# Performance work log

Hardware: AMD Instinct MI355X
Metric: run time of the kernel (lower is better)

Reference implementation:

```python
import jax, jax.numpy as jnp
import numpy as np

B, S, D, F, E = 8, 2048, 512, 2048, 8


def setup_inputs() -> dict:
    key = jax.random.key(0)
    ks = jax.random.split(key, 7)
    x = jax.random.normal(ks[0], (B, S, D), dtype=jnp.float32)
    Wr = jax.random.normal(ks[1], (D, E), dtype=jnp.float32) * 0.02
    br = jnp.zeros((E,), dtype=jnp.float32)
    W1 = jax.random.normal(ks[2], (E, D, F), dtype=jnp.float32) * 0.02
    b1 = jnp.zeros((E, F), dtype=jnp.float32)
    W2 = jax.random.normal(ks[3], (E, F, D), dtype=jnp.float32) * 0.02
    b2 = jnp.zeros((E, D), dtype=jnp.float32)
    return {"x": x, "Wr": Wr, "br": br, "W1": W1, "b1": b1, "W2": W2, "b2": b2}


def reference(x, Wr, br, W1, b1, W2, b2):
    # Router: softmax gate + top-2
    logits = jnp.einsum('bsd,de->bse', x, Wr) + br            # [B,S,E]
    gate = jax.nn.softmax(logits, axis=-1)                    # [B,S,E]
    top2_val, top2_idx = jax.lax.top_k(gate, 2)               # [B,S,2]

    # Combine weights: gate value on the two selected experts, 0 elsewhere
    onehot = jax.nn.one_hot(top2_idx, E, dtype=x.dtype)       # [B,S,2,E]
    combine = jnp.sum(onehot * top2_val[..., None], axis=2)   # [B,S,E]

    # Dense per-expert FFN, masked-combined (same math as the token loop)
    out = jnp.zeros_like(x)
    for e in range(E):
        h = jax.nn.relu(jnp.einsum('bsd,df->bsf', x, W1[e]) + b1[e])
        y = jnp.einsum('bsf,fd->bsd', h, W2[e]) + b2[e]
        out = out + combine[..., e, None] * y

    # GShard-style load-balancing aux loss
    expert_prob = gate.mean(axis=(0, 1))                      # [E]
    aux_loss = jnp.sum(expert_prob * jnp.log(expert_prob + 1e-9))
    return out, aux_loss
```

## Files before the change

kernel.cpp:

```cpp
#include <hip/hip_runtime.h>
#include <math.h>

typedef unsigned short u16;
typedef __attribute__((ext_vector_type(8))) short short8;
typedef __attribute__((ext_vector_type(8))) u16 u16x8;
typedef __attribute__((ext_vector_type(4))) float f32x4;

#define NTOK 16384
#define DDIM 512
#define FDIM 2048
#define ENUM 8
#define NBLK 1024
#define APAD (32768 + 256)
#define MAXTILES 264

__device__ __forceinline__ u16 f2bf(float f) {
  unsigned u = __float_as_uint(f);
  u += 0x7FFFu + ((u >> 16) & 1u);
  return (u16)(u >> 16);
}
__device__ __forceinline__ float bf2f(u16 b) {
  return __uint_as_float(((unsigned)b) << 16);
}

typedef const __attribute__((address_space(1))) unsigned int* gas1_t;
typedef __attribute__((address_space(3))) unsigned int* las3_t;
__device__ __forceinline__ void gload16(const u16* g, u16* l) {
  __builtin_amdgcn_global_load_lds((gas1_t)(const void*)g, (las3_t)(void*)l, 16, 0, 0);
}

__global__ __launch_bounds__(256) void router_kernel(
    const float* __restrict__ x, const float* __restrict__ Wr,
    const float* __restrict__ br, int* __restrict__ top2e,
    float* __restrict__ top2v, int* __restrict__ histBase,
    float* __restrict__ gatePart) {
  __shared__ __align__(16) float sWr[DDIM * ENUM];
  __shared__ __align__(16) float sX[4][DDIM];
  __shared__ int sHist[ENUM];
  __shared__ float sGate[ENUM];
  int tid = threadIdx.x;
  for (int i = tid; i < DDIM * ENUM; i += 256) sWr[i] = Wr[i];
  if (tid < ENUM) { sHist[tid] = 0; sGate[tid] = 0.f; }
  __syncthreads();
  int wave = tid >> 6, lane = tid & 63;
  int e = lane >> 3, dg = lane & 7;
  float bre = br[e];
  for (int it = 0; it < 4; ++it) {
    int t = blockIdx.x * 16 + wave * 4 + it;
    const float4* xr = (const float4*)(x + (size_t)t * DDIM);
    float4* sx4 = (float4*)sX[wave];
    sx4[lane] = xr[lane];
    sx4[lane + 64] = xr[lane + 64];
    asm volatile("s_waitcnt lgkmcnt(0)" ::: "memory");
    float acc = 0.f;
#pragma unroll 16
    for (int i = 0; i < 64; ++i) {
      float xv = sX[wave][i * 8 + dg];
      acc += xv * sWr[(i * 8 + dg) * 8 + e];
    }
    acc += __shfl_xor(acc, 1);
    acc += __shfl_xor(acc, 2);
    acc += __shfl_xor(acc, 4);
    float logit = acc + bre;
    float m = logit;
    m = fmaxf(m, __shfl_xor(m, 8));
    m = fmaxf(m, __shfl_xor(m, 16));
    m = fmaxf(m, __shfl_xor(m, 32));
    float pv = expf(logit - m);
    float s = pv;
    s += __shfl_xor(s, 8);
    s += __shfl_xor(s, 16);
    s += __shfl_xor(s, 32);
    float gate = pv / s;
    float v1 = gate; int i1 = e;
#pragma unroll
    for (int msk = 8; msk <= 32; msk <<= 1) {
      float ov = __shfl_xor(v1, msk);
      int oi = __shfl_xor(i1, msk);
      if (ov > v1 || (ov == v1 && oi < i1)) { v1 = ov; i1 = oi; }
    }
    float g2 = (e == i1) ? -1.f : gate;
    float v2 = g2; int i2 = e;
#pragma unroll
    for (int msk = 8; msk <= 32; msk <<= 1) {
      float ov = __shfl_xor(v2, msk);
      int oi = __shfl_xor(i2, msk);
      if (ov > v2 || (ov == v2 && oi < i2)) { v2 = ov; i2 = oi; }
    }
    if (lane == 0) {
      top2e[2 * t] = i1; top2e[2 * t + 1] = i2;
      top2v[2 * t] = v1; top2v[2 * t + 1] = v2;
      atomicAdd(&sHist[i1], 1);
      atomicAdd(&sHist[i2], 1);
    }
    if (dg == 0) atomicAdd(&sGate[e], gate);
  }
  __syncthreads();
  if (tid < ENUM) {
    histBase[blockIdx.x * 8 + tid] = sHist[tid];
    gatePart[blockIdx.x * 8 + tid] = sGate[tid];
  }
}

__global__ __launch_bounds__(256) void scan_kernel(
    int* __restrict__ histBase, const float* __restrict__ gatePart,
    int* __restrict__ offsets, int* __restrict__ counts,
    int* __restrict__ tileE, int* __restrict__ tileM, int* __restrict__ nTiles,
    float* __restrict__ auxOut) {
  __shared__ int sTot[ENUM];
  __shared__ float sG[ENUM];
  int tid = threadIdx.x, wave = tid >> 6, lane = tid & 63;
  if (tid < ENUM) sG[tid] = 0.f;
  __syncthreads();
  float loc[8] = {0, 0, 0, 0, 0, 0, 0, 0};
  for (int r = tid; r < NBLK; r += 256) {
#pragma unroll
    for (int e = 0; e < 8; ++e) loc[e] += gatePart[r * 8 + e];
  }
#pragma unroll
  for (int e = 0; e < 8; ++e) atomicAdd(&sG[e], loc[e]);
#pragma unroll
  for (int ei = 0; ei < 2; ++ei) {
    int e = wave * 2 + ei;
    int running = 0;
    for (int itb = 0; itb < NBLK / 64; ++itb) {
      int idx = (itb * 64 + lane) * 8 + e;
      int v = histBase[idx];
      int inc = v;
#pragma unroll
      for (int d = 1; d < 64; d <<= 1) {
        int o = __shfl_up(inc, d);
        if (lane >= d) inc += o;
      }
      histBase[idx] = running + inc - v;
      running += __shfl(inc, 63);
    }
    if (lane == 0) sTot[e] = running;
  }
  __syncthreads();
  if (tid == 0) {
    int off = 0, nt = 0;
#pragma unroll
    for (int e = 0; e < 8; ++e) {
      int c = sTot[e];
      offsets[e] = off; counts[e] = c; off += c;
      int mt = (c + 127) >> 7;
      for (int m = 0; m < mt; ++m) { tileE[nt] = e; tileM[nt] = m; ++nt; }
    }
    *nTiles = nt;
    float aux = 0.f;
#pragma unroll
    for (int e = 0; e < 8; ++e) {
      float pr = sG[e] / (float)NTOK;
      aux += pr * logf(pr + 1e-9f);
    }
    *auxOut = aux;
  }
}

__global__ __launch_bounds__(256) void place_kernel(
    const float* __restrict__ x, const int* __restrict__ top2e,
    const float* __restrict__ top2v, const int* __restrict__ histBase,
    const int* __restrict__ offsets, int* __restrict__ tokA,
    float* __restrict__ assignW, u16* __restrict__ Xg) {
  __shared__ int sA[32];
  int tid = threadIdx.x, wave = tid >> 6, lane = tid & 63;
  int blk = blockIdx.x;
  if (tid < 32) {
    int slot = tid;
    int t = blk * 16 + (slot >> 1);
    int e = top2e[2 * t + (slot & 1)];
    float v = top2v[2 * t + (slot & 1)];
    int rank = 0;
#pragma unroll
    for (int ee = 0; ee < 8; ++ee) {
      unsigned long long mm = __ballot(e == ee);
      if (e == ee) rank = __popcll(mm & ((1ull << slot) - 1));
    }
    int a = offsets[e] + histBase[blk * 8 + e] + rank;
    sA[slot] = a;
    tokA[2 * t + (slot & 1)] = a;
    assignW[a] = v;
  }
  __syncthreads();
  for (int it = 0; it < 4; ++it) {
    int lt = wave * 4 + it;
    int t = blk * 16 + lt;
    const float4* xr = (const float4*)(x + (size_t)t * DDIM);
    float4 v0 = xr[lane * 2], v1 = xr[lane * 2 + 1];
    u16x8 o;
    o[0] = f2bf(v0.x); o[1] = f2bf(v0.y); o[2] = f2bf(v0.z); o[3] = f2bf(v0.w);
    o[4] = f2bf(v1.x); o[5] = f2bf(v1.y); o[6] = f2bf(v1.z); o[7] = f2bf(v1.w);
    int a1 = sA[2 * lt], a2 = sA[2 * lt + 1];
    *(u16x8*)(Xg + (size_t)a1 * DDIM + lane * 8) = o;
    *(u16x8*)(Xg + (size_t)a2 * DDIM + lane * 8) = o;
  }
}

__global__ __launch_bounds__(256) void transpose_kernel(
    const float* __restrict__ W, u16* __restrict__ WT, int K, int N) {
  __shared__ float tile[64][65];
  int e = blockIdx.y;
  int tn_count = N >> 6;
  int tk = blockIdx.x / tn_count;
  int tn = blockIdx.x - tk * tn_count;
  const float* Wp = W + (size_t)e * K * N;
  u16* WTp = WT + (size_t)e * N * K;
  int c = threadIdx.x & 63, r = threadIdx.x >> 6;
#pragma unroll
  for (int i = 0; i < 16; ++i) {
    int row = r + i * 4;
    tile[row][c] = Wp[(size_t)(tk * 64 + row) * N + tn * 64 + c];
  }
  __syncthreads();
#pragma unroll
  for (int i = 0; i < 16; ++i) {
    int row = r + i * 4;
    WTp[(size_t)(tn * 64 + row) * K + tk * 64 + c] = f2bf(tile[c][row]);
  }
}

template <int K>
__device__ __forceinline__ void gemm_mainloop(const u16* __restrict__ A,
                                              const u16* __restrict__ B,
                                              u16* As, u16* Bs,
                                              f32x4 (&acc)[4][4]) {
  int tid = threadIdx.x;
  int wave = tid >> 6, lane = tid & 63;
  int wr = wave >> 1, wc = wave & 1;
  int c0 = tid, c1 = tid + 256;
  int r0 = c0 >> 2, r1 = c1 >> 2;
  int f0 = (r0 ^ (r0 >> 2)) & 3;
  int k0c = ((c0 & 3) ^ f0) * 8;
  int k1c = ((c1 & 3) ^ f0) * 8;
  const u16* Ag0 = A + (size_t)r0 * K + k0c;
  const u16* Ag1 = A + (size_t)r1 * K + k1c;
  const u16* Bg0 = B + (size_t)r0 * K + k0c;
  const u16* Bg1 = B + (size_t)r1 * K + k1c;
  int wb = wave * 512;
  int fr = lane & 15;
  int sw = (fr ^ (fr >> 2)) & 3;
  int slot = (lane >> 4) ^ sw;
  int fA = (wr * 64 + fr) * 32 + slot * 8;
  int fB = (wc * 64 + fr) * 32 + slot * 8;

  gload16(Ag0, As + wb);
  gload16(Ag1, As + 2048 + wb);
  gload16(Bg0, Bs + wb);
  gload16(Bg1, Bs + 2048 + wb);
  __syncthreads();
  int cur = 0;
  for (int k0 = 32; k0 < K; k0 += 32) {
    int nb = (cur ^ 1) * 4096;
    gload16(Ag0 + k0, As + nb + wb);
    gload16(Ag1 + k0, As + nb + 2048 + wb);
    gload16(Bg0 + k0, Bs + nb + wb);
    gload16(Bg1 + k0, Bs + nb + 2048 + wb);
    const u16* Ac = As + cur * 4096;
    const u16* Bc = Bs + cur * 4096;
    short8 af[4], bf[4];
#pragma unroll
    for (int m = 0; m < 4; ++m) af[m] = *(const short8*)(Ac + fA + m * 512);
#pragma unroll
    for (int n = 0; n < 4; ++n) bf[n] = *(const short8*)(Bc + fB + n * 512);
#pragma unroll
    for (int m = 0; m < 4; ++m)
#pragma unroll
      for (int n = 0; n < 4; ++n)
        acc[m][n] = __builtin_amdgcn_mfma_f32_16x16x32_bf16(af[m], bf[n],
                                                            acc[m][n], 0, 0, 0);
    __syncthreads();
    cur ^= 1;
  }
  const u16* Ac = As + cur * 4096;
  const u16* Bc = Bs + cur * 4096;
  short8 af[4], bf[4];
#pragma unroll
  for (int m = 0; m < 4; ++m) af[m] = *(const short8*)(Ac + fA + m * 512);
#pragma unroll
  for (int n = 0; n < 4; ++n) bf[n] = *(const short8*)(Bc + fB + n * 512);
#pragma unroll
  for (int m = 0; m < 4; ++m)
#pragma unroll
    for (int n = 0; n < 4; ++n)
      acc[m][n] = __builtin_amdgcn_mfma_f32_16x16x32_bf16(af[m], bf[n],
                                                          acc[m][n], 0, 0, 0);
}

__global__ __launch_bounds__(256) void gemm1_kernel(
    const u16* __restrict__ Xg, const u16* __restrict__ W1T,
    const float* __restrict__ b1, u16* __restrict__ h,
    const int* __restrict__ counts, const int* __restrict__ offsets,
    const int* __restrict__ tileE, const int* __restrict__ tileM,
    const int* __restrict__ nTiles) {
  if ((int)blockIdx.x >= *nTiles) return;
  int e = tileE[blockIdx.x], mtile = tileM[blockIdx.x];
  int ntile = blockIdx.y;
  int cnt = counts[e], off = offsets[e];
  const u16* A = Xg + (size_t)(off + mtile * 128) * DDIM;
  const u16* B = W1T + ((size_t)e * FDIM + ntile * 128) * DDIM;
  __shared__ __align__(16) u16 As[2 * 128 * 32];
  __shared__ __align__(16) u16 Bs[2 * 128 * 32];
  f32x4 acc[4][4] = {};
  gemm_mainloop<DDIM>(A, B, As, Bs, acc);
  int lane = threadIdx.x & 63, wave = threadIdx.x >> 6;
  int wr = wave >> 1, wc = wave & 1;
  int cl = lane & 15, rq = (lane >> 4) * 4;
#pragma unroll
  for (int m = 0; m < 4; ++m) {
#pragma unroll
    for (int i = 0; i < 4; ++i) {
      int gr = mtile * 128 + wr * 64 + m * 16 + rq + i;
      if (gr < cnt) {
#pragma unroll
        for (int n = 0; n < 4; ++n) {
          int gc = ntile * 128 + wc * 64 + n * 16 + cl;
          float v = acc[m][n][i] + b1[e * FDIM + gc];
          v = fmaxf(v, 0.f);
          h[(size_t)(off + gr) * FDIM + gc] = f2bf(v);
        }
      }
    }
  }
}

__global__ __launch_bounds__(256) void gemm2_kernel(
    const u16* __restrict__ h, const u16* __restrict__ W2T,
    const float* __restrict__ b2, const float* __restrict__ assignW,
    const int* __restrict__ counts, const int* __restrict__ offsets,
    const int* __restrict__ tileE, const int* __restrict__ tileM,
    const int* __restrict__ nTiles, u16* __restrict__ z) {
  if ((int)blockIdx.x >= *nTiles) return;
  int e = tileE[blockIdx.x], mtile = tileM[blockIdx.x];
  int ntile = blockIdx.y;
  int cnt = counts[e], off = offsets[e];
  const u16* A = h + (size_t)(off + mtile * 128) * FDIM;
  const u16* B = W2T + ((size_t)e * DDIM + ntile * 128) * FDIM;
  __shared__ __align__(16) u16 As[2 * 128 * 32];
  __shared__ __align__(16) u16 Bs[2 * 128 * 32];
  f32x4 acc[4][4] = {};
  gemm_mainloop<FDIM>(A, B, As, Bs, acc);
  int lane = threadIdx.x & 63, wave = threadIdx.x >> 6;
  int wr = wave >> 1, wc = wave & 1;
  int cl = lane & 15, rq = (lane >> 4) * 4;
#pragma unroll
  for (int m = 0; m < 4; ++m) {
#pragma unroll
    for (int i = 0; i < 4; ++i) {
      int gr = mtile * 128 + wr * 64 + m * 16 + rq + i;
      if (gr < cnt) {
        int a = off + gr;
        float w = assignW[a];
#pragma unroll
        for (int n = 0; n < 4; ++n) {
          int gc = ntile * 128 + wc * 64 + n * 16 + cl;
          float v = (acc[m][n][i] + b2[e * DDIM + gc]) * w;
          z[(size_t)a * DDIM + gc] = f2bf(v);
        }
      }
    }
  }
}

__global__ __launch_bounds__(256) void combine_kernel(
    const u16* __restrict__ z, const int* __restrict__ tokA,
    float* __restrict__ out) {
  int tid = threadIdx.x, wave = tid >> 6, lane = tid & 63;
  int t = blockIdx.x * 4 + wave;
  int a1 = tokA[2 * t], a2 = tokA[2 * t + 1];
  u16x8 v1 = *(const u16x8*)(z + (size_t)a1 * DDIM + lane * 8);
  u16x8 v2 = *(const u16x8*)(z + (size_t)a2 * DDIM + lane * 8);
  float4 o0, o1;
  o0.x = bf2f(v1[0]) + bf2f(v2[0]);
  o0.y = bf2f(v1[1]) + bf2f(v2[1]);
  o0.z = bf2f(v1[2]) + bf2f(v2[2]);
  o0.w = bf2f(v1[3]) + bf2f(v2[3]);
  o1.x = bf2f(v1[4]) + bf2f(v2[4]);
  o1.y = bf2f(v1[5]) + bf2f(v2[5]);
  o1.z = bf2f(v1[6]) + bf2f(v2[6]);
  o1.w = bf2f(v1[7]) + bf2f(v2[7]);
  float4* o = (float4*)(out + (size_t)t * DDIM + lane * 8);
  o[0] = o0;
  o[1] = o1;
}

extern "C" void kernel_launch(void* const* d_in, const int* in_sizes, int n_in,
                              void* d_out, int out_size, void* d_ws, size_t ws_size,
                              hipStream_t stream) {
  const float* x  = (const float*)d_in[0];
  const float* Wr = (const float*)d_in[1];
  const float* br = (const float*)d_in[2];
  const float* W1 = (const float*)d_in[3];
  const float* b1 = (const float*)d_in[4];
  const float* W2 = (const float*)d_in[5];
  const float* b2 = (const float*)d_in[6];
  float* out = (float*)d_out;

  char* ws = (char*)d_ws;
  size_t p = 0;
  auto alloc = [&](size_t bytes) -> void* {
    void* r = ws + p;
    p = (p + bytes + 255) & ~(size_t)255;
    return r;
  };
  int* counts     = (int*)alloc(ENUM * 4);
  int* offsets    = (int*)alloc(ENUM * 4);
  int* nTiles     = (int*)alloc(4);
  int* tileE      = (int*)alloc(MAXTILES * 4);
  int* tileM      = (int*)alloc(MAXTILES * 4);
  int* top2e      = (int*)alloc((size_t)NTOK * 2 * 4);
  float* top2v    = (float*)alloc((size_t)NTOK * 2 * 4);
  int* tokA       = (int*)alloc((size_t)NTOK * 2 * 4);
  float* assignW  = (float*)alloc((size_t)APAD * 4);
  int* histBase   = (int*)alloc((size_t)NBLK * 8 * 4);
  float* gatePart = (float*)alloc((size_t)NBLK * 8 * 4);
  u16* W1T        = (u16*)alloc((size_t)ENUM * FDIM * DDIM * 2);
  u16* W2T        = (u16*)alloc((size_t)ENUM * DDIM * FDIM * 2);
  u16* Xg         = (u16*)alloc((size_t)APAD * DDIM * 2);
  u16* hbuf       = (u16*)alloc((size_t)APAD * FDIM * 2);
  u16* z          = Xg;
  (void)in_sizes; (void)n_in; (void)out_size; (void)ws_size;

  transpose_kernel<<<dim3(256, 8), 256, 0, stream>>>(W1, W1T, DDIM, FDIM);
  transpose_kernel<<<dim3(256, 8), 256, 0, stream>>>(W2, W2T, FDIM, DDIM);
  router_kernel<<<NBLK, 256, 0, stream>>>(x, Wr, br, top2e, top2v, histBase,
                                          gatePart);
  scan_kernel<<<1, 256, 0, stream>>>(histBase, gatePart, offsets, counts,
                                     tileE, tileM, nTiles,
                                     out + (size_t)NTOK * DDIM);
  place_kernel<<<NBLK, 256, 0, stream>>>(x, top2e, top2v, histBase, offsets,
                                         tokA, assignW, Xg);
  gemm1_kernel<<<dim3(MAXTILES, 16), 256, 0, stream>>>(
      Xg, W1T, b1, hbuf, counts, offsets, tileE, tileM, nTiles);
  gemm2_kernel<<<dim3(MAXTILES, 4), 256, 0, stream>>>(
      hbuf, W2T, b2, assignW, counts, offsets, tileE, tileM, nTiles, z);
  combine_kernel<<<NTOK / 4, 256, 0, stream>>>(z, tokA, out);
}
```

Before: 348.0 us.

## Rewrite expert GEMMs as 256x256 tiles with 8-wave ping-pong pipelined mainloop

Replaces the 128x128 double-buffered GEMM mainloop with a 256x256 tile kernel using 512 threads and 128KB of dynamic LDS. The new loop is a phased schedule: it splits A and B into K-halves, interleaves global-to-LDS loads with MFMA bursts, and uses explicit barriers, waitcnt and setprio to overlap memory with compute. Each tile's operands are reused more and there are fewer blocks. The cost is more padding waste for experts whose token counts are not multiples of 256, fewer blocks to fill the CUs, and one block per CU.

New measurement: 327.8 us. 5.8% less time.

```diff
diff --git a/kernel.cpp b/kernel.cpp
--- a/kernel.cpp
+++ b/kernel.cpp
@@ -12,7 +12,7 @@
 #define ENUM 8
 #define NBLK 1024
 #define APAD (32768 + 256)
-#define MAXTILES 264
+#define MAXT 144
 
 __device__ __forceinline__ u16 f2bf(float f) {
   unsigned u = __float_as_uint(f);
@@ -144,7 +144,7 @@
     for (int e = 0; e < 8; ++e) {
       int c = sTot[e];
       offsets[e] = off; counts[e] = c; off += c;
-      int mt = (c + 127) >> 7;
+      int mt = (c + 255) >> 8;
       for (int m = 0; m < mt; ++m) { tileE[nt] = e; tileM[nt] = m; ++nt; }
     }
     *nTiles = nt;
@@ -220,102 +220,120 @@
   }
 }
 
+
+#define STG(SP0, SP1, SOP, SBUF, SKH, SKT)                                     \
+  do {                                                                         \
+    const size_t go_ = (size_t)(SKT) * 64 + (SKH) * 32;                        \
+    gload16((SP0) + go_, (u16*)(ldsB + (SOP) * 65536 + (SBUF) * 32768 +        \
+                                (SKH) * 16384 + w1024));                       \
+    gload16((SP1) + go_, (u16*)(ldsB + (SOP) * 65536 + (SBUF) * 32768 +        \
+                                (SKH) * 16384 + 8192 + w1024));                \
+  } while (0)
+
+#define PH(MH, KS, CBUF, SP0, SP1, SOP, SBUF, SKH, SKT, GATE)                  \
+  do {                                                                         \
+    short8 areg[4];                                                            \
+    _Pragma("unroll")                                                          \
+    for (int m_ = 0; m_ < 4; ++m_)                                             \
+      areg[m_] = *(const short8*)(ldsB + (CBUF) * 32768 + (KS) * 16384 +       \
+                                  (MH) * 4096 + m_ * 1024 + frA);              \
+    if ((MH) == 0) {                                                           \
+      _Pragma("unroll")                                                        \
+      for (int n_ = 0; n_ < 4; ++n_)                                           \
+        breg[n_] = *(const short8*)(ldsB + 65536 + (CBUF) * 32768 +            \
+                                    (KS) * 16384 + n_ * 1024 + frB);           \
+    }                                                                          \
+    STG(SP0, SP1, SOP, SBUF, SKH, SKT);                                        \
+    if (GATE) asm volatile("s_waitcnt vmcnt(8)" ::: "memory");                 \
+    __builtin_amdgcn_s_barrier();                                              \
+    __builtin_amdgcn_sched_barrier(0);                                         \
+    __builtin_amdgcn_s_setprio(1);                                             \
+    _Pragma("unroll")                                                          \
+    for (int m_ = 0; m_ < 4; ++m_)                                             \
+      _Pragma("unroll")                                                        \
+      for (int n_ = 0; n_ < 4; ++n_)                                           \
+        acc[(MH) * 4 + m_][n_] = __builtin_amdgcn_mfma_f32_16x16x32_bf16(      \
+            areg[m_], breg[n_], acc[(MH) * 4 + m_][n_], 0, 0, 0);              \
+    __builtin_amdgcn_s_setprio(0);                                             \
+    __builtin_amdgcn_s_barrier();                                              \
+    __builtin_amdgcn_sched_barrier(0);                                         \
+  } while (0)
+
 template <int K>
-__device__ __forceinline__ void gemm_mainloop(const u16* __restrict__ A,
-                                              const u16* __restrict__ B,
-                                              u16* As, u16* Bs,
-                                              f32x4 (&acc)[4][4]) {
-  int tid = threadIdx.x;
-  int wave = tid >> 6, lane = tid & 63;
-  int wr = wave >> 1, wc = wave & 1;
-  int c0 = tid, c1 = tid + 256;
-  int r0 = c0 >> 2, r1 = c1 >> 2;
-  int f0 = (r0 ^ (r0 >> 2)) & 3;
-  int k0c = ((c0 & 3) ^ f0) * 8;
-  int k1c = ((c1 & 3) ^ f0) * 8;
-  const u16* Ag0 = A + (size_t)r0 * K + k0c;
-  const u16* Ag1 = A + (size_t)r1 * K + k1c;
-  const u16* Bg0 = B + (size_t)r0 * K + k0c;
-  const u16* Bg1 = B + (size_t)r1 * K + k1c;
-  int wb = wave * 512;
-  int fr = lane & 15;
-  int sw = (fr ^ (fr >> 2)) & 3;
-  int slot = (lane >> 4) ^ sw;
-  int fA = (wr * 64 + fr) * 32 + slot * 8;
-  int fB = (wc * 64 + fr) * 32 + slot * 8;
-
-  gload16(Ag0, As + wb);
-  gload16(Ag1, As + 2048 + wb);
-  gload16(Bg0, Bs + wb);
-  gload16(Bg1, Bs + 2048 + wb);
-  __syncthreads();
-  int cur = 0;
-  for (int k0 = 32; k0 < K; k0 += 32) {
-    int nb = (cur ^ 1) * 4096;
-    gload16(Ag0 + k0, As + nb + wb);
-    gload16(Ag1 + k0, As + nb + 2048 + wb);
-    gload16(Bg0 + k0, Bs + nb + wb);
-    gload16(Bg1 + k0, Bs + nb + 2048 + wb);
-    const u16* Ac = As + cur * 4096;
-    const u16* Bc = Bs + cur * 4096;
-    short8 af[4], bf[4];
-#pragma unroll
-    for (int m = 0; m < 4; ++m) af[m] = *(const short8*)(Ac + fA + m * 512);
-#pragma unroll
-    for (int n = 0; n < 4; ++n) bf[n] = *(const short8*)(Bc + fB + n * 512);
-#pragma unroll
-    for (int m = 0; m < 4; ++m)
-#pragma unroll
-      for (int n = 0; n < 4; ++n)
-        acc[m][n] = __builtin_amdgcn_mfma_f32_16x16x32_bf16(af[m], bf[n],
-                                                            acc[m][n], 0, 0, 0);
-    __syncthreads();
-    cur ^= 1;
-  }
-  const u16* Ac = As + cur * 4096;
-  const u16* Bc = Bs + cur * 4096;
-  short8 af[4], bf[4];
-#pragma unroll
-  for (int m = 0; m < 4; ++m) af[m] = *(const short8*)(Ac + fA + m * 512);
-#pragma unroll
-  for (int n = 0; n < 4; ++n) bf[n] = *(const short8*)(Bc + fB + n * 512);
-#pragma unroll
-  for (int m = 0; m < 4; ++m)
-#pragma unroll
-    for (int n = 0; n < 4; ++n)
-      acc[m][n] = __builtin_amdgcn_mfma_f32_16x16x32_bf16(af[m], bf[n],
-                                                          acc[m][n], 0, 0, 0);
-}
-
-__global__ __launch_bounds__(256) void gemm1_kernel(
+__device__ __forceinline__ void mainloop8(const u16* __restrict__ A,
+                                          const u16* __restrict__ B,
+                                          char* ldsB, f32x4 (&acc)[8][4]) {
+  const int tid = threadIdx.x;
+  const int lane = tid & 63, wave = tid >> 6;
+  const int wr = wave >> 2, wc = wave & 3;
+  const int fr = lane & 15;
+  const int swzRd = (((lane >> 4) ^ ((lane >> 1) & 3)) & 3) * 16;
+  const int frA = (wr * 128 + fr) * 64 + swzRd;
+  const int frB = (wc * 64 + fr) * 64 + swzRd;
+  const int w1024 = wave * 1024;
+  const int rowS = wave * 16 + (lane >> 2);
+  const int cswz = ((lane & 3) ^ ((lane >> 3) & 3)) * 8;
+  const u16* bA0 = A + (size_t)rowS * K + cswz;
+  const u16* bA1 = A + (size_t)(rowS + 128) * K + cswz;
+  const u16* bB0 = B + (size_t)rowS * K + cswz;
+  const u16* bB1 = B + (size_t)(rowS + 128) * K + cswz;
+  const int KT = K / 64, NIT = KT / 2;
+  short8 breg[4];
+
+  STG(bA0, bA1, 0, 0, 0, 0);
+  STG(bB0, bB1, 1, 0, 0, 0);
+  STG(bA0, bA1, 0, 0, 1, 0);
+  STG(bB0, bB1, 1, 0, 1, 0);
+  STG(bA0, bA1, 0, 1, 0, 1);
+  STG(bB0, bB1, 1, 1, 0, 1);
+  asm volatile("s_waitcnt vmcnt(8)" ::: "memory");
+  __builtin_amdgcn_s_barrier();
+  __builtin_amdgcn_sched_barrier(0);
+
+#pragma unroll 1
+  for (int it = 0; it < NIT; ++it) {
+    const int t1 = 2 * it + 1;
+    const int t2 = (2 * it + 2) & (KT - 1);
+    const int t3 = (2 * it + 3) & (KT - 1);
+    PH(0, 0, 0, bA0, bA1, 0, 1, 1, t1, 0);
+    PH(1, 0, 0, bB0, bB1, 1, 1, 1, t1, 1);
+    PH(0, 1, 0, bA0, bA1, 0, 0, 0, t2, 0);
+    PH(1, 1, 0, bB0, bB1, 1, 0, 0, t2, 1);
+    PH(0, 0, 1, bA0, bA1, 0, 0, 1, t2, 0);
+    PH(1, 0, 1, bB0, bB1, 1, 0, 1, t2, 1);
+    PH(0, 1, 1, bA0, bA1, 0, 1, 0, t3, 0);
+    PH(1, 1, 1, bB0, bB1, 1, 1, 0, t3, 1);
+  }
+}
+
+__global__ __launch_bounds__(512, 1) void gemm1_kernel(
     const u16* __restrict__ Xg, const u16* __restrict__ W1T,
     const float* __restrict__ b1, u16* __restrict__ h,
     const int* __restrict__ counts, const int* __restrict__ offsets,
     const int* __restrict__ tileE, const int* __restrict__ tileM,
     const int* __restrict__ nTiles) {
+  extern __shared__ char ldsB[];
   if ((int)blockIdx.x >= *nTiles) return;
   int e = tileE[blockIdx.x], mtile = tileM[blockIdx.x];
   int ntile = blockIdx.y;
   int cnt = counts[e], off = offsets[e];
-  const u16* A = Xg + (size_t)(off + mtile * 128) * DDIM;
-  const u16* B = W1T + ((size_t)e * FDIM + ntile * 128) * DDIM;
-  __shared__ __align__(16) u16 As[2 * 128 * 32];
-  __shared__ __align__(16) u16 Bs[2 * 128 * 32];
-  f32x4 acc[4][4] = {};
-  gemm_mainloop<DDIM>(A, B, As, Bs, acc);
+  const u16* A = Xg + (size_t)(off + mtile * 256) * DDIM;
+  const u16* B = W1T + ((size_t)e * FDIM + ntile * 256) * DDIM;
+  f32x4 acc[8][4] = {};
+  mainloop8<DDIM>(A, B, ldsB, acc);
   int lane = threadIdx.x & 63, wave = threadIdx.x >> 6;
-  int wr = wave >> 1, wc = wave & 1;
+  int wr = wave >> 2, wc = wave & 3;
   int cl = lane & 15, rq = (lane >> 4) * 4;
 #pragma unroll
-  for (int m = 0; m < 4; ++m) {
+  for (int ai = 0; ai < 8; ++ai) {
 #pragma unroll
     for (int i = 0; i < 4; ++i) {
-      int gr = mtile * 128 + wr * 64 + m * 16 + rq + i;
+      int gr = mtile * 256 + wr * 128 + ai * 16 + rq + i;
       if (gr < cnt) {
 #pragma unroll
         for (int n = 0; n < 4; ++n) {
-          int gc = ntile * 128 + wc * 64 + n * 16 + cl;
-          float v = acc[m][n][i] + b1[e * FDIM + gc];
+          int gc = ntile * 256 + wc * 64 + n * 16 + cl;
+          float v = acc[ai][n][i] + b1[e * FDIM + gc];
           v = fmaxf(v, 0.f);
           h[(size_t)(off + gr) * FDIM + gc] = f2bf(v);
         }
@@ -324,37 +342,36 @@
   }
 }
 
-__global__ __launch_bounds__(256) void gemm2_kernel(
+__global__ __launch_bounds__(512, 1) void gemm2_kernel(
     const u16* __restrict__ h, const u16* __restrict__ W2T,
     const float* __restrict__ b2, const float* __restrict__ assignW,
     const int* __restrict__ counts, const int* __restrict__ offsets,
     const int* __restrict__ tileE, const int* __restrict__ tileM,
     const int* __restrict__ nTiles, u16* __restrict__ z) {
+  extern __shared__ char ldsB[];
   if ((int)blockIdx.x >= *nTiles) return;
   int e = tileE[blockIdx.x], mtile = tileM[blockIdx.x];
   int ntile = blockIdx.y;
   int cnt = counts[e], off = offsets[e];
-  const u16* A = h + (size_t)(off + mtile * 128) * FDIM;
-  const u16* B = W2T + ((size_t)e * DDIM + ntile * 128) * FDIM;
-  __shared__ __align__(16) u16 As[2 * 128 * 32];
-  __shared__ __align__(16) u16 Bs[2 * 128 * 32];
-  f32x4 acc[4][4] = {};
-  gemm_mainloop<FDIM>(A, B, As, Bs, acc);
+  const u16* A = h + (size_t)(off + mtile * 256) * FDIM;
+  const u16* B = W2T + ((size_t)e * DDIM + ntile * 256) * FDIM;
+  f32x4 acc[8][4] = {};
+  mainloop8<FDIM>(A, B, ldsB, acc);
   int lane = threadIdx.x & 63, wave = threadIdx.x >> 6;
-  int wr = wave >> 1, wc = wave & 1;
+  int wr = wave >> 2, wc = wave & 3;
   int cl = lane & 15, rq = (lane >> 4) * 4;
 #pragma unroll
-  for (int m = 0; m < 4; ++m) {
+  for (int ai = 0; ai < 8; ++ai) {
 #pragma unroll
     for (int i = 0; i < 4; ++i) {
-      int gr = mtile * 128 + wr * 64 + m * 16 + rq + i;
+      int gr = mtile * 256 + wr * 128 + ai * 16 + rq + i;
       if (gr < cnt) {
         int a = off + gr;
         float w = assignW[a];
 #pragma unroll
         for (int n = 0; n < 4; ++n) {
-          int gc = ntile * 128 + wc * 64 + n * 16 + cl;
-          float v = (acc[m][n][i] + b2[e * DDIM + gc]) * w;
+          int gc = ntile * 256 + wc * 64 + n * 16 + cl;
+          float v = (acc[ai][n][i] + b2[e * DDIM + gc]) * w;
           z[(size_t)a * DDIM + gc] = f2bf(v);
         }
       }
@@ -406,8 +423,8 @@
   int* counts     = (int*)alloc(ENUM * 4);
   int* offsets    = (int*)alloc(ENUM * 4);
   int* nTiles     = (int*)alloc(4);
-  int* tileE      = (int*)alloc(MAXTILES * 4);
-  int* tileM      = (int*)alloc(MAXTILES * 4);
+  int* tileE      = (int*)alloc(MAXT * 4);
+  int* tileM      = (int*)alloc(MAXT * 4);
   int* top2e      = (int*)alloc((size_t)NTOK * 2 * 4);
   float* top2v    = (float*)alloc((size_t)NTOK * 2 * 4);
   int* tokA       = (int*)alloc((size_t)NTOK * 2 * 4);
@@ -421,6 +438,11 @@
   u16* z          = Xg;
   (void)in_sizes; (void)n_in; (void)out_size; (void)ws_size;
 
+  (void)hipFuncSetAttribute((const void*)gemm1_kernel,
+                            hipFuncAttributeMaxDynamicSharedMemorySize, 131072);
+  (void)hipFuncSetAttribute((const void*)gemm2_kernel,
+                            hipFuncAttributeMaxDynamicSharedMemorySize, 131072);
+
   transpose_kernel<<<dim3(256, 8), 256, 0, stream>>>(W1, W1T, DDIM, FDIM);
   transpose_kernel<<<dim3(256, 8), 256, 0, stream>>>(W2, W2T, FDIM, DDIM);
   router_kernel<<<NBLK, 256, 0, stream>>>(x, Wr, br, top2e, top2v, histBase,
@@ -430,9 +452,9 @@
                                      out + (size_t)NTOK * DDIM);
   place_kernel<<<NBLK, 256, 0, stream>>>(x, top2e, top2v, histBase, offsets,
                                          tokA, assignW, Xg);
-  gemm1_kernel<<<dim3(MAXTILES, 16), 256, 0, stream>>>(
+  gemm1_kernel<<<dim3(MAXT, 8), 512, 131072, stream>>>(
       Xg, W1T, b1, hbuf, counts, offsets, tileE, tileM, nTiles);
-  gemm2_kernel<<<dim3(MAXTILES, 4), 256, 0, stream>>>(
+  gemm2_kernel<<<dim3(MAXT, 2), 512, 131072, stream>>>(
       hbuf, W2T, b2, assignW, counts, offsets, tileE, tileM, nTiles, z);
   combine_kernel<<<NTOK / 4, 256, 0, stream>>>(z, tokA, out);
 }
```

## Widen GEMM tiles to 128x256 with 8 waves, remap grid, fuse transposes

Applied to the files above, without the earlier changes.

Both expert GEMMs now use 512-thread workgroups computing 128x256 output tiles, so each A tile in LDS is reused across twice as many columns and fewer A loads are issued overall. The 2D grid becomes a 1D grid with an XCD-aware block remap, MFMA sections are wrapped in s_setprio, and launch bounds request higher occupancy. The two weight-transpose launches are merged into one kernel using float4 loads and 16-byte bf16 stores. The trade-off is larger LDS per block and more wasted columns or threads on partially filled expert tiles.

Result: slower. 1.181 ms (+239.3%).

```diff
diff --git a/kernel.cpp b/kernel.cpp
--- a/kernel.cpp
+++ b/kernel.cpp
@@ -12,7 +12,9 @@
 #define ENUM 8
 #define NBLK 1024
 #define APAD (32768 + 256)
-#define MAXTILES 264
+#define NTCAP 264
+#define G1GRID 2112
+#define G2GRID 528
 
 __device__ __forceinline__ u16 f2bf(float f) {
   unsigned u = __float_as_uint(f);
@@ -105,7 +107,7 @@
 __global__ __launch_bounds__(256) void scan_kernel(
     int* __restrict__ histBase, const float* __restrict__ gatePart,
     int* __restrict__ offsets, int* __restrict__ counts,
-    int* __restrict__ tileE, int* __restrict__ tileM, int* __restrict__ nTiles,
+    int* __restrict__ tileE, int* __restrict__ tileM, int* __restrict__ nT,
     float* __restrict__ auxOut) {
   __shared__ int sTot[ENUM];
   __shared__ float sG[ENUM];
@@ -147,7 +149,7 @@
       int mt = (c + 127) >> 7;
       for (int m = 0; m < mt; ++m) { tileE[nt] = e; tileM[nt] = m; ++nt; }
     }
-    *nTiles = nt;
+    nT[0] = nt;
     float aux = 0.f;
 #pragma unroll
     for (int e = 0; e < 8; ++e) {
@@ -198,113 +200,125 @@
 }
 
 __global__ __launch_bounds__(256) void transpose_kernel(
-    const float* __restrict__ W, u16* __restrict__ WT, int K, int N) {
+    const float* __restrict__ W1, const float* __restrict__ W2,
+    u16* __restrict__ W1T, u16* __restrict__ W2T) {
   __shared__ float tile[64][65];
-  int e = blockIdx.y;
-  int tn_count = N >> 6;
-  int tk = blockIdx.x / tn_count;
-  int tn = blockIdx.x - tk * tn_count;
-  const float* Wp = W + (size_t)e * K * N;
-  u16* WTp = WT + (size_t)e * N * K;
-  int c = threadIdx.x & 63, r = threadIdx.x >> 6;
-#pragma unroll
-  for (int i = 0; i < 16; ++i) {
-    int row = r + i * 4;
-    tile[row][c] = Wp[(size_t)(tk * 64 + row) * N + tn * 64 + c];
-  }
-  __syncthreads();
-#pragma unroll
-  for (int i = 0; i < 16; ++i) {
-    int row = r + i * 4;
-    WTp[(size_t)(tn * 64 + row) * K + tk * 64 + c] = f2bf(tile[c][row]);
+  int q = threadIdx.x;
+  int half = blockIdx.y >> 3, e = blockIdx.y & 7;
+  const float* W = half ? W2 : W1;
+  u16* WT = half ? W2T : W1T;
+  int K = half ? FDIM : DDIM, N = half ? DDIM : FDIM;
+  int tnc = N >> 6;
+  int tk = blockIdx.x / tnc, tn = blockIdx.x - tk * tnc;
+  const float* Wp = W + (size_t)e * K * N + (size_t)(tk * 64) * N + tn * 64;
+#pragma unroll
+  for (int i = 0; i < 4; ++i) {
+    int row = (q >> 4) + i * 16, c4 = (q & 15) * 4;
+    float4 v = *(const float4*)(Wp + (size_t)row * N + c4);
+    tile[row][c4] = v.x; tile[row][c4 + 1] = v.y;
+    tile[row][c4 + 2] = v.z; tile[row][c4 + 3] = v.w;
+  }
+  __syncthreads();
+  u16* WTp = WT + (size_t)e * N * K + (size_t)(tn * 64) * K + tk * 64;
+#pragma unroll
+  for (int p = 0; p < 2; ++p) {
+    int n = (q >> 3) + p * 32, k0 = (q & 7) * 8;
+    u16x8 o;
+#pragma unroll
+    for (int j = 0; j < 8; ++j) o[j] = f2bf(tile[k0 + j][n]);
+    *(u16x8*)(WTp + (size_t)n * K + k0) = o;
   }
 }
 
 template <int K>
-__device__ __forceinline__ void gemm_mainloop(const u16* __restrict__ A,
-                                              const u16* __restrict__ B,
-                                              u16* As, u16* Bs,
-                                              f32x4 (&acc)[4][4]) {
-  int tid = threadIdx.x;
-  int wave = tid >> 6, lane = tid & 63;
-  int wr = wave >> 1, wc = wave & 1;
-  int c0 = tid, c1 = tid + 256;
-  int r0 = c0 >> 2, r1 = c1 >> 2;
-  int f0 = (r0 ^ (r0 >> 2)) & 3;
-  int k0c = ((c0 & 3) ^ f0) * 8;
-  int k1c = ((c1 & 3) ^ f0) * 8;
-  const u16* Ag0 = A + (size_t)r0 * K + k0c;
-  const u16* Ag1 = A + (size_t)r1 * K + k1c;
-  const u16* Bg0 = B + (size_t)r0 * K + k0c;
-  const u16* Bg1 = B + (size_t)r1 * K + k1c;
-  int wb = wave * 512;
-  int fr = lane & 15;
-  int sw = (fr ^ (fr >> 2)) & 3;
-  int slot = (lane >> 4) ^ sw;
-  int fA = (wr * 64 + fr) * 32 + slot * 8;
-  int fB = (wc * 64 + fr) * 32 + slot * 8;
-
-  gload16(Ag0, As + wb);
-  gload16(Ag1, As + 2048 + wb);
-  gload16(Bg0, Bs + wb);
-  gload16(Bg1, Bs + 2048 + wb);
-  __syncthreads();
+__device__ __forceinline__ void mainloopS(const u16* __restrict__ A,
+                                          const u16* __restrict__ B,
+                                          u16* As, u16* Bs,
+                                          f32x4 (&acc)[4][4]) {
+  const int tid = threadIdx.x;
+  const int lane = tid & 63, wave = tid >> 6;
+  const int wr = wave >> 2, wc = wave & 3;
+  const int fr = lane & 15;
+  const int slot = ((lane >> 4) ^ (fr ^ (fr >> 2))) & 3;
+  const int frA = (wr * 64 + fr) * 32 + slot * 8;
+  const int frB = (wc * 64 + fr) * 32 + slot * 8;
+  const int rA = tid >> 2;
+  const int sA = (((tid & 3) ^ (rA ^ (rA >> 2))) & 3) * 8;
+  const u16* Ag = A + (size_t)rA * K + sA;
+  const u16* Bg0 = B + (size_t)rA * K + sA;
+  const u16* Bg1 = B + (size_t)(rA + 128) * K + sA;
+  u16* Adst = As + wave * 512;
+  u16* Bdst0 = Bs + wave * 512;
+  u16* Bdst1 = Bs + 4096 + wave * 512;
+  const int KT = K / 32;
+
+  gload16(Ag, Adst);
+  gload16(Bg0, Bdst0);
+  gload16(Bg1, Bdst1);
+  __syncthreads();
+
   int cur = 0;
-  for (int k0 = 32; k0 < K; k0 += 32) {
-    int nb = (cur ^ 1) * 4096;
-    gload16(Ag0 + k0, As + nb + wb);
-    gload16(Ag1 + k0, As + nb + 2048 + wb);
-    gload16(Bg0 + k0, Bs + nb + wb);
-    gload16(Bg1 + k0, Bs + nb + 2048 + wb);
+#pragma unroll 1
+  for (int ks = 0; ks < KT - 1; ++ks) {
+    const int nb = cur ^ 1;
+    gload16(Ag + (ks + 1) * 32, Adst + nb * 4096);
+    gload16(Bg0 + (ks + 1) * 32, Bdst0 + nb * 8192);
+    gload16(Bg1 + (ks + 1) * 32, Bdst1 + nb * 8192);
     const u16* Ac = As + cur * 4096;
-    const u16* Bc = Bs + cur * 4096;
+    const u16* Bc = Bs + cur * 8192;
     short8 af[4], bf[4];
 #pragma unroll
-    for (int m = 0; m < 4; ++m) af[m] = *(const short8*)(Ac + fA + m * 512);
-#pragma unroll
-    for (int n = 0; n < 4; ++n) bf[n] = *(const short8*)(Bc + fB + n * 512);
+    for (int m = 0; m < 4; ++m) af[m] = *(const short8*)(Ac + frA + m * 512);
+#pragma unroll
+    for (int n = 0; n < 4; ++n) bf[n] = *(const short8*)(Bc + frB + n * 512);
+    __builtin_amdgcn_s_setprio(1);
 #pragma unroll
     for (int m = 0; m < 4; ++m)
 #pragma unroll
       for (int n = 0; n < 4; ++n)
         acc[m][n] = __builtin_amdgcn_mfma_f32_16x16x32_bf16(af[m], bf[n],
                                                             acc[m][n], 0, 0, 0);
+    __builtin_amdgcn_s_setprio(0);
     __syncthreads();
-    cur ^= 1;
-  }
-  const u16* Ac = As + cur * 4096;
-  const u16* Bc = Bs + cur * 4096;
-  short8 af[4], bf[4];
-#pragma unroll
-  for (int m = 0; m < 4; ++m) af[m] = *(const short8*)(Ac + fA + m * 512);
-#pragma unroll
-  for (int n = 0; n < 4; ++n) bf[n] = *(const short8*)(Bc + fB + n * 512);
-#pragma unroll
-  for (int m = 0; m < 4; ++m)
-#pragma unroll
-    for (int n = 0; n < 4; ++n)
-      acc[m][n] = __builtin_amdgcn_mfma_f32_16x16x32_bf16(af[m], bf[n],
-                                                          acc[m][n], 0, 0, 0);
-}
-
-__global__ __launch_bounds__(256) void gemm1_kernel(
+    cur = nb;
+  }
+  {
+    const u16* Ac = As + cur * 4096;
+    const u16* Bc = Bs + cur * 8192;
+    short8 af[4], bf[4];
+#pragma unroll
+    for (int m = 0; m < 4; ++m) af[m] = *(const short8*)(Ac + frA + m * 512);
+#pragma unroll
+    for (int n = 0; n < 4; ++n) bf[n] = *(const short8*)(Bc + frB + n * 512);
+#pragma unroll
+    for (int m = 0; m < 4; ++m)
+#pragma unroll
+      for (int n = 0; n < 4; ++n)
+        acc[m][n] = __builtin_amdgcn_mfma_f32_16x16x32_bf16(af[m], bf[n],
+                                                            acc[m][n], 0, 0, 0);
+  }
+}
+
+__global__ __launch_bounds__(512, 6) void gemm1_kernel(
     const u16* __restrict__ Xg, const u16* __restrict__ W1T,
     const float* __restrict__ b1, u16* __restrict__ h,
     const int* __restrict__ counts, const int* __restrict__ offsets,
     const int* __restrict__ tileE, const int* __restrict__ tileM,
-    const int* __restrict__ nTiles) {
-  if ((int)blockIdx.x >= *nTiles) return;
-  int e = tileE[blockIdx.x], mtile = tileM[blockIdx.x];
-  int ntile = blockIdx.y;
+    const int* __restrict__ nT) {
+  __shared__ __align__(16) u16 As[2 * 128 * 32];
+  __shared__ __align__(16) u16 Bs[2 * 256 * 32];
+  int wg = blockIdx.x;
+  int L = (wg & 7) * (G1GRID / 8) + (wg >> 3);
+  int tile = L >> 3, ntile = L & 7;
+  if (tile >= nT[0]) return;
+  int e = tileE[tile], mtile = tileM[tile];
   int cnt = counts[e], off = offsets[e];
   const u16* A = Xg + (size_t)(off + mtile * 128) * DDIM;
-  const u16* B = W1T + ((size_t)e * FDIM + ntile * 128) * DDIM;
-  __shared__ __align__(16) u16 As[2 * 128 * 32];
-  __shared__ __align__(16) u16 Bs[2 * 128 * 32];
+  const u16* B = W1T + ((size_t)e * FDIM + ntile * 256) * DDIM;
   f32x4 acc[4][4] = {};
-  gemm_mainloop<DDIM>(A, B, As, Bs, acc);
+  mainloopS<DDIM>(A, B, As, Bs, acc);
   int lane = threadIdx.x & 63, wave = threadIdx.x >> 6;
-  int wr = wave >> 1, wc = wave & 1;
+  int wr = wave >> 2, wc = wave & 3;
   int cl = lane & 15, rq = (lane >> 4) * 4;
 #pragma unroll
   for (int m = 0; m < 4; ++m) {
@@ -314,7 +328,7 @@
       if (gr < cnt) {
 #pragma unroll
         for (int n = 0; n < 4; ++n) {
-          int gc = ntile * 128 + wc * 64 + n * 16 + cl;
+          int gc = ntile * 256 + wc * 64 + n * 16 + cl;
           float v = acc[m][n][i] + b1[e * FDIM + gc];
           v = fmaxf(v, 0.f);
           h[(size_t)(off + gr) * FDIM + gc] = f2bf(v);
@@ -324,24 +338,26 @@
   }
 }
 
-__global__ __launch_bounds__(256) void gemm2_kernel(
+__global__ __launch_bounds__(512, 6) void gemm2_kernel(
     const u16* __restrict__ h, const u16* __restrict__ W2T,
     const float* __restrict__ b2, const float* __restrict__ assignW,
     const int* __restrict__ counts, const int* __restrict__ offsets,
     const int* __restrict__ tileE, const int* __restrict__ tileM,
-    const int* __restrict__ nTiles, u16* __restrict__ z) {
-  if ((int)blockIdx.x >= *nTiles) return;
-  int e = tileE[blockIdx.x], mtile = tileM[blockIdx.x];
-  int ntile = blockIdx.y;
+    const int* __restrict__ nT, u16* __restrict__ z) {
+  __shared__ __align__(16) u16 As[2 * 128 * 32];
+  __shared__ __align__(16) u16 Bs[2 * 256 * 32];
+  int wg = blockIdx.x;
+  int L = (wg & 7) * (G2GRID / 8) + (wg >> 3);
+  int tile = L >> 1, ntile = L & 1;
+  if (tile >= nT[0]) return;
+  int e = tileE[tile], mtile = tileM[tile];
   int cnt = counts[e], off = offsets[e];
   const u16* A = h + (size_t)(off + mtile * 128) * FDIM;
-  const u16* B = W2T + ((size_t)e * DDIM + ntile * 128) * FDIM;
-  __shared__ __align__(16) u16 As[2 * 128 * 32];
-  __shared__ __align__(16) u16 Bs[2 * 128 * 32];
+  const u16* B = W2T + ((size_t)e * DDIM + ntile * 256) * FDIM;
   f32x4 acc[4][4] = {};
-  gemm_mainloop<FDIM>(A, B, As, Bs, acc);
+  mainloopS<FDIM>(A, B, As, Bs, acc);
   int lane = threadIdx.x & 63, wave = threadIdx.x >> 6;
-  int wr = wave >> 1, wc = wave & 1;
+  int wr = wave >> 2, wc = wave & 3;
   int cl = lane & 15, rq = (lane >> 4) * 4;
 #pragma unroll
   for (int m = 0; m < 4; ++m) {
@@ -353,7 +369,7 @@
         float w = assignW[a];
 #pragma unroll
         for (int n = 0; n < 4; ++n) {
-          int gc = ntile * 128 + wc * 64 + n * 16 + cl;
+          int gc = ntile * 256 + wc * 64 + n * 16 + cl;
           float v = (acc[m][n][i] + b2[e * DDIM + gc]) * w;
           z[(size_t)a * DDIM + gc] = f2bf(v);
         }
@@ -405,9 +421,9 @@
   };
   int* counts     = (int*)alloc(ENUM * 4);
   int* offsets    = (int*)alloc(ENUM * 4);
-  int* nTiles     = (int*)alloc(4);
-  int* tileE      = (int*)alloc(MAXTILES * 4);
-  int* tileM      = (int*)alloc(MAXTILES * 4);
+  int* nT         = (int*)alloc(4);
+  int* tileE      = (int*)alloc(NTCAP * 4);
+  int* tileM      = (int*)alloc(NTCAP * 4);
   int* top2e      = (int*)alloc((size_t)NTOK * 2 * 4);
   float* top2v    = (float*)alloc((size_t)NTOK * 2 * 4);
   int* tokA       = (int*)alloc((size_t)NTOK * 2 * 4);
@@ -421,18 +437,17 @@
   u16* z          = Xg;
   (void)in_sizes; (void)n_in; (void)out_size; (void)ws_size;
 
-  transpose_kernel<<<dim3(256, 8), 256, 0, stream>>>(W1, W1T, DDIM, FDIM);
-  transpose_kernel<<<dim3(256, 8), 256, 0, stream>>>(W2, W2T, FDIM, DDIM);
+  transpose_kernel<<<dim3(256, 16), 256, 0, stream>>>(W1, W2, W1T, W2T);
   router_kernel<<<NBLK, 256, 0, stream>>>(x, Wr, br, top2e, top2v, histBase,
                                           gatePart);
   scan_kernel<<<1, 256, 0, stream>>>(histBase, gatePart, offsets, counts,
-                                     tileE, tileM, nTiles,
+                                     tileE, tileM, nT,
                                      out + (size_t)NTOK * DDIM);
   place_kernel<<<NBLK, 256, 0, stream>>>(x, top2e, top2v, histBase, offsets,
                                          tokA, assignW, Xg);
-  gemm1_kernel<<<dim3(MAXTILES, 16), 256, 0, stream>>>(
-      Xg, W1T, b1, hbuf, counts, offsets, tileE, tileM, nTiles);
-  gemm2_kernel<<<dim3(MAXTILES, 4), 256, 0, stream>>>(
-      hbuf, W2T, b2, assignW, counts, offsets, tileE, tileM, nTiles, z);
+  gemm1_kernel<<<G1GRID, 512, 0, stream>>>(
+      Xg, W1T, b1, hbuf, counts, offsets, tileE, tileM, nT);
+  gemm2_kernel<<<G2GRID, 512, 0, stream>>>(
+      hbuf, W2T, b2, assignW, counts, offsets, tileE, tileM, nT, z);
   combine_kernel<<<NTOK / 4, 256, 0, stream>>>(z, tokA, out);
 }
```
